# Kernel optimization log

Measured on AMD Instinct MI355X. Metric: run time of the kernel, lower is better.

The kernel has to match this reference:

```python
import jax, jax.numpy as jnp
import numpy as np
import math

B, T, C = 8, 1024, 512
H = 8
HD = C // H  # 64
MAX_REL = 64 + 4  # args.block_size + args.time_cond


def setup_inputs() -> dict:
    key = jax.random.key(0)
    ks = jax.random.split(key, 12)
    xavier = lambda k, shape: jax.random.uniform(
        k, shape, jnp.float32, -1.0, 1.0) * math.sqrt(6.0 / (shape[0] + shape[1]))
    return {
        "x": jax.random.normal(ks[0], (B, T, C), jnp.float32),
        "Wq": xavier(ks[1], (C, C)), "bq": jnp.zeros((C,), jnp.float32),
        "Wk": xavier(ks[2], (C, C)), "bk": jnp.zeros((C,), jnp.float32),
        "Wv": xavier(ks[3], (C, C)), "bv": jnp.zeros((C,), jnp.float32),
        "Wo": xavier(ks[4], (C, C)), "bo": jnp.zeros((C,), jnp.float32),
        "rel_k": xavier(ks[5], (2 * MAX_REL + 1, HD)),
        "rel_v": xavier(ks[6], (2 * MAX_REL + 1, HD)),
    }


def _rel_index(t):
    # clipped relative distance matrix, shifted to [0, 2*MAX_REL]
    r = jnp.arange(t)
    dist = jnp.clip(r[None, :] - r[:, None], -MAX_REL, MAX_REL)
    return dist + MAX_REL  # (T, T) int32


def reference(x, Wq, bq, Wk, bk, Wv, bv, Wo, bo, rel_k, rel_v):
    b, t, c = x.shape
    h, hd = H, HD
    q = x @ Wq + bq
    k = x @ Wk + bk
    v = x @ Wv + bv
    rq = q.reshape(b, t, h, hd).transpose(0, 2, 1, 3)  # (B,H,T,hd)
    rk = k.reshape(b, t, h, hd).transpose(0, 2, 1, 3)
    rv = v.reshape(b, t, h, hd).transpose(0, 2, 1, 3)

    idx = _rel_index(t)                 # (T,T)
    rk2 = rel_k[idx]                    # (T,T,hd)
    rv2 = rel_v[idx]                    # (T,T,hd)

    attn1 = jnp.einsum("bhqd,bhkd->bhqk", rq, rk)
    attn2 = jnp.einsum("bhqd,qkd->bhqk", rq, rk2)
    # NOTE: original scales by 1/sqrt(embed_dim) (k.size(-1) == C), not head_dim
    attn = jax.nn.softmax((attn1 + attn2) * (1.0 / math.sqrt(c)), axis=-1)

    w1 = jnp.einsum("bhqk,bhkd->bhqd", attn, rv)
    w2 = jnp.einsum("bhqk,qkd->bhqd", attn, rv2)
    out = (w1 + w2).transpose(0, 2, 1, 3).reshape(b, t, c)
    return out @ Wo + bo
```

## Files before the change

### kernel.cpp

```cpp
#include <hip/hip_runtime.h>
#include <stdint.h>

#define Bb 8
#define Tt 1024
#define Cc 512
#define Hh 8
#define HD 64
#define MREL 68
#define NR 137
#define NRP 160
#define SCALE 0.044194173824159216f
#define KSCL  0.063763016845703125f

typedef unsigned short u16;
typedef unsigned int u32;
using u16x4  = __attribute__((ext_vector_type(4))) u16;
using u16x8  = __attribute__((ext_vector_type(8))) u16;
using u32x4  = __attribute__((ext_vector_type(4))) u32;
using f32x4  = __attribute__((ext_vector_type(4))) float;
using f32x16 = __attribute__((ext_vector_type(16))) float;
using bf16x8 = __attribute__((ext_vector_type(8))) __bf16;

__device__ __forceinline__ u16 f2bf(float f) {
  u32 u = __builtin_bit_cast(u32, f);
  u += 0x7FFF + ((u >> 16) & 1);
  return (u16)(u >> 16);
}
__device__ __forceinline__ float bf2f(u16 v) {
  return __builtin_bit_cast(float, (u32)v << 16);
}
__device__ __forceinline__ bf16x8 as_bf8(u16x8 v) { return __builtin_bit_cast(bf16x8, v); }
__device__ __forceinline__ bf16x8 frag4(u32 w0, u32 w1, u32 w2, u32 w3) {
  u32x4 v = {w0, w1, w2, w3};
  return __builtin_bit_cast(bf16x8, v);
}
__device__ __forceinline__ float fexp2(float x) {
  float r; asm("v_exp_f32 %0, %1" : "=v"(r) : "v"(x)); return r;
}
__device__ __forceinline__ u32 cvtpk(float lo, float hi) {
  u32 r; asm("v_cvt_pk_bf16_f32 %0, %1, %2" : "=v"(r) : "v"(lo), "v"(hi)); return r;
}
__device__ __forceinline__ bf16x8 ldsplit(const u16* base) {
  u16x4 lo = *(const u16x4*)(base);
  u16x4 hi = *(const u16x4*)(base + 8);
  u16x8 r = {lo[0], lo[1], lo[2], lo[3], hi[0], hi[1], hi[2], hi[3]};
  return as_bf8(r);
}

#define MFMA16(a, b, c) __builtin_amdgcn_mfma_f32_16x16x32_bf16((a), (b), (c), 0, 0, 0)
#define MFMA32(a, b, c) __builtin_amdgcn_mfma_f32_32x32x16_bf16((a), (b), (c), 0, 0, 0)

__global__ __launch_bounds__(256) void relv_prep(
    const float* __restrict__ rel_v, u16* __restrict__ rvT)
{
  int i = blockIdx.x * 256 + threadIdx.x;
  if (i < HD * NRP) {
    int d = i / NRP, r = i - d * NRP;
    rvT[i] = (r < NR) ? f2bf(rel_v[r * HD + d]) : (u16)0;
  }
}

__global__ __launch_bounds__(256) void w_prep(
    const float* __restrict__ Wq, const float* __restrict__ Wk,
    const float* __restrict__ Wv, const float* __restrict__ Wo,
    u16* __restrict__ WqT, u16* __restrict__ WkT,
    u16* __restrict__ WvT, u16* __restrict__ WoT)
{
  const float* W = blockIdx.y == 0 ? Wq : blockIdx.y == 1 ? Wk
                  : blockIdx.y == 2 ? Wv : Wo;
  u16* WT = blockIdx.y == 0 ? WqT : blockIdx.y == 1 ? WkT
           : blockIdx.y == 2 ? WvT : WoT;
  int i = blockIdx.x * 256 + threadIdx.x;
  int n = i >> 7, k4 = (i & 127) * 4;
  u16x4 o;
  #pragma unroll
  for (int j = 0; j < 4; ++j) o[j] = f2bf(W[(size_t)(k4 + j) * Cc + n]);
  *(u16x4*)&WT[(size_t)n * Cc + k4] = o;
}

__global__ __launch_bounds__(256) void qkv_gemm(
    const float* __restrict__ x,
    const u16* __restrict__ WqT, const u16* __restrict__ WkT,
    const u16* __restrict__ WvT,
    const float* __restrict__ bq, const float* __restrict__ bk,
    const float* __restrict__ bv,
    u16* __restrict__ Qb, u16* __restrict__ Kb, u16* __restrict__ VTb)
{
  __shared__ u16 Xs[64][40];
  __shared__ u16 WTs[3][64][40];

  const u16* Wp[3] = {WqT, WkT, WvT};
  const float* bp[3] = {bq, bk, bv};

  const int tid = threadIdx.x;
  const int wv_ = tid >> 6;
  const int l   = tid & 63;
  const int lr  = l & 15, lg = l >> 4;
  const int m0  = blockIdx.x * 64;
  const int n0  = blockIdx.y * 64;
  const int srow = tid >> 2, scol = (tid & 3) * 8;

  f32x4 acc[3][4];
  #pragma unroll
  for (int a = 0; a < 3; ++a)
    #pragma unroll
    for (int b = 0; b < 4; ++b) acc[a][b] = (f32x4){0.f, 0.f, 0.f, 0.f};

  for (int k0 = 0; k0 < Cc; k0 += 32) {
    {
      const float* xp = x + (size_t)(m0 + srow) * Cc + k0 + scol;
      f32x4 v0 = *(const f32x4*)xp;
      f32x4 v1 = *(const f32x4*)(xp + 4);
      u16x8 o = {f2bf(v0[0]), f2bf(v0[1]), f2bf(v0[2]), f2bf(v0[3]),
                 f2bf(v1[0]), f2bf(v1[1]), f2bf(v1[2]), f2bf(v1[3])};
      *(u16x8*)&Xs[srow][scol] = o;
    }
    #pragma unroll
    for (int q3 = 0; q3 < 3; ++q3) {
      u16x8 w = *(const u16x8*)(Wp[q3] + (size_t)(n0 + srow) * Cc + k0 + scol);
      *(u16x8*)&WTs[q3][srow][scol] = w;
    }
    __syncthreads();

    bf16x8 a = as_bf8(*(const u16x8*)&Xs[wv_ * 16 + lr][lg * 8]);
    #pragma unroll
    for (int q3 = 0; q3 < 3; ++q3) {
      #pragma unroll
      for (int nt = 0; nt < 4; ++nt) {
        bf16x8 b = as_bf8(*(const u16x8*)&WTs[q3][nt * 16 + lr][lg * 8]);
        acc[q3][nt] = MFMA16(a, b, acc[q3][nt]);
      }
    }
    __syncthreads();
  }

  const int bidx = m0 >> 10;
  #pragma unroll
  for (int q3 = 0; q3 < 3; ++q3) {
    #pragma unroll
    for (int nt = 0; nt < 4; ++nt) {
      int n = n0 + nt * 16 + lr;
      int h = n >> 6, d = n & 63;
      float bias = bp[q3][n];
      #pragma unroll
      for (int i = 0; i < 4; ++i) {
        int m = m0 + wv_ * 16 + lg * 4 + i;
        int t = m & (Tt - 1);
        u16 o = f2bf(acc[q3][nt][i] + bias);
        size_t bh = (size_t)(bidx * Hh + h);
        if (q3 == 0)      Qb[(bh * Tt + t) * HD + d] = o;
        else if (q3 == 1) Kb[(bh * Tt + t) * HD + d] = o;
        else              VTb[(bh * HD + d) * Tt + t] = o;
      }
    }
  }
}

__global__ __launch_bounds__(256, 3) void attn_kernel(
    const u16* __restrict__ Qb, const u16* __restrict__ Kb,
    const u16* __restrict__ VTb, const u16* __restrict__ rvT,
    const float* __restrict__ rel_k,
    u16* __restrict__ AO)
{
  __shared__ u16 S2L[32][144];
  __shared__ u16 a2L[32][176];
  __shared__ float Obuf[32][64];
  __shared__ float red[3][4][32];
  __shared__ float rowrcp[32];

  const int tid = threadIdx.x;
  const int wv_ = tid >> 6, l = tid & 63;
  const int l31 = l & 31, hi = l >> 5;
  const int lr16 = l & 15, lg16 = l >> 4;
  const int bh = blockIdx.x;
  const int q0 = blockIdx.y * 32;
  const int bidx = bh >> 3, h = bh & 7;

  const u16* Qh = Qb  + (size_t)bh * Tt * HD;
  const u16* Kh = Kb  + (size_t)bh * Tt * HD;
  const u16* Vh = VTb + (size_t)bh * HD * Tt;

  for (int i = tid; i < 32 * 176 / 2; i += 256) ((u32*)a2L)[i] = 0;
  for (int i = tid; i < 32 * 64; i += 256) ((float*)Obuf)[i] = 0.f;

  #pragma unroll
  for (int h16 = 0; h16 < 2; ++h16) {
    bf16x8 aQ0 = as_bf8(*(const u16x8*)(Qh + (size_t)(q0 + h16 * 16 + lr16) * HD + lg16 * 8));
    bf16x8 aQ1 = as_bf8(*(const u16x8*)(Qh + (size_t)(q0 + h16 * 16 + lr16) * HD + 32 + lg16 * 8));
    for (int ct = wv_; ct < 9; ct += 4) {
      int r = ct * 16 + lr16;
      f32x4 acc = {0.f, 0.f, 0.f, 0.f};
      #pragma unroll
      for (int d0 = 0; d0 < 64; d0 += 32) {
        u16x8 bbits = {0, 0, 0, 0, 0, 0, 0, 0};
        if (r < NR) {
          f32x4 v0 = *(const f32x4*)(rel_k + (size_t)r * HD + d0 + lg16 * 8);
          f32x4 v1 = *(const f32x4*)(rel_k + (size_t)r * HD + d0 + lg16 * 8 + 4);
          bbits = (u16x8){f2bf(v0[0]), f2bf(v0[1]), f2bf(v0[2]), f2bf(v0[3]),
                          f2bf(v1[0]), f2bf(v1[1]), f2bf(v1[2]), f2bf(v1[3])};
        }
        acc = MFMA16(d0 ? aQ1 : aQ0, as_bf8(bbits), acc);
      }
      #pragma unroll
      for (int i = 0; i < 4; ++i)
        S2L[h16 * 16 + lg16 * 4 + i][ct * 16 + lr16] = f2bf(acc[i] * KSCL);
    }
  }
  __syncthreads();

  const int qme = q0 + l31;
  const float cN = bf2f(S2L[l31][0]);
  const float cP = bf2f(S2L[l31][NR - 1]);

  bf16x8 qf[4];
  #pragma unroll
  for (int s = 0; s < 4; ++s)
    qf[s] = as_bf8(*(const u16x8*)(Qh + (size_t)qme * HD + 16 * s + 8 * hi));

  const int wk0 = wv_ * 256;
  f32x16 oA = {}, oB = {};
  float ps = 0.f, ps0 = 0.f, bnd = 0.f;

  #pragma unroll
  for (int t = 0; t < 8; ++t) {
    const int kc0 = wk0 + 32 * t;
    bf16x8 kf[4];
    #pragma unroll
    for (int s = 0; s < 4; ++s)
      kf[s] = as_bf8(*(const u16x8*)(Kh + (size_t)(kc0 + l31) * HD + 16 * s + 8 * hi));

    f32x16 acc = {};
    #pragma unroll
    for (int s = 0; s < 4; ++s) acc = MFMA32(kf[s], qf[s], acc);

    float p[16];
    const bool isLow  = (kc0 <= q0 - 99);
    const bool isHigh = (kc0 >= q0 + 99);
    if (isLow | isHigh) {
      const float c = isLow ? cN : cP;
      #pragma unroll
      for (int r = 0; r < 16; ++r) p[r] = fexp2(fmaf(acc[r], KSCL, c));
      float s16 = ((p[0]+p[1])+(p[2]+p[3])) + ((p[4]+p[5])+(p[6]+p[7]))
                + ((p[8]+p[9])+(p[10]+p[11])) + ((p[12]+p[13])+(p[14]+p[15]));
      ps += s16;
      if (isLow) ps0 += s16;
    } else {
      #pragma unroll
      for (int r = 0; r < 16; ++r) {
        int kcoff = (r & 3) + 8 * (r >> 2) + 4 * hi;
        int dr = kc0 + kcoff - qme;
        int drc = dr < -MREL ? -MREL : (dr > MREL ? MREL : dr);
        float pe = fexp2(fmaf(acc[r], KSCL, bf2f(S2L[l31][drc + MREL])));
        p[r] = pe;
        ps += pe;
        if (dr <= -MREL) ps0 += pe;
        if (dr >= -67 && dr <= 67) { a2L[l31][dr + MREL] = f2bf(pe); bnd += pe; }
      }
    }

    bf16x8 paLo = frag4(cvtpk(p[0], p[1]),  cvtpk(p[2], p[3]),
                        cvtpk(p[4], p[5]),  cvtpk(p[6], p[7]));
    bf16x8 paHi = frag4(cvtpk(p[8], p[9]),  cvtpk(p[10], p[11]),
                        cvtpk(p[12], p[13]), cvtpk(p[14], p[15]));

    const u16* vA = Vh + (size_t)l31 * Tt;
    const u16* vB = Vh + (size_t)(32 + l31) * Tt;
    bf16x8 vA0 = ldsplit(vA + kc0 + 4 * hi);
    bf16x8 vA1 = ldsplit(vA + kc0 + 16 + 4 * hi);
    bf16x8 vB0 = ldsplit(vB + kc0 + 4 * hi);
    bf16x8 vB1 = ldsplit(vB + kc0 + 16 + 4 * hi);
    oA = MFMA32(paLo, vA0, oA);
    oA = MFMA32(paHi, vA1, oA);
    oB = MFMA32(paLo, vB0, oB);
    oB = MFMA32(paHi, vB1, oB);
  }

  ps  += __shfl_xor(ps, 32);
  ps0 += __shfl_xor(ps0, 32);
  bnd += __shfl_xor(bnd, 32);
  if (l < 32) { red[0][wv_][l] = ps; red[1][wv_][l] = ps0; red[2][wv_][l] = bnd; }
  __syncthreads();

  if (tid < 32) {
    float t0 = red[0][0][tid] + red[0][1][tid] + red[0][2][tid] + red[0][3][tid];
    float t1 = red[1][0][tid] + red[1][1][tid] + red[1][2][tid] + red[1][3][tid];
    float tb = red[2][0][tid] + red[2][1][tid] + red[2][2][tid] + red[2][3][tid];
    a2L[tid][0]      = f2bf(t1);
    a2L[tid][NR - 1] = f2bf(t0 - t1 - tb);
    rowrcp[tid] = 1.0f / t0;
  }
  __syncthreads();

  for (int W = wv_; W < 10; W += 4) {
    bf16x8 aa = as_bf8(*(const u16x8*)&a2L[l31][W * 16 + 8 * hi]);
    bf16x8 rA = as_bf8(*(const u16x8*)(rvT + (size_t)l31 * NRP        + W * 16 + 8 * hi));
    bf16x8 rB = as_bf8(*(const u16x8*)(rvT + (size_t)(32 + l31) * NRP + W * 16 + 8 * hi));
    oA = MFMA32(aa, rA, oA);
    oB = MFMA32(aa, rB, oB);
  }

  #pragma unroll
  for (int r = 0; r < 16; ++r) {
    int qoff = (r & 3) + 8 * (r >> 2) + 4 * hi;
    atomicAdd(&Obuf[qoff][l31], oA[r]);
    atomicAdd(&Obuf[qoff][32 + l31], oB[r]);
  }
  __syncthreads();

  {
    int rq = tid >> 3, d8 = (tid & 7) * 8;
    float rc = rowrcp[rq];
    u16x8 o;
    #pragma unroll
    for (int j = 0; j < 8; ++j) o[j] = f2bf(Obuf[rq][d8 + j] * rc);
    *(u16x8*)&AO[((size_t)(bidx * Tt + q0 + rq)) * Cc + h * HD + d8] = o;
  }
}

__global__ __launch_bounds__(256) void out_gemm(
    const u16* __restrict__ AO, const u16* __restrict__ WoT,
    const float* __restrict__ bo, float* __restrict__ out)
{
  __shared__ u16 As[64][40];
  __shared__ u16 WTs[64][40];
  const int tid = threadIdx.x;
  const int wv_ = tid >> 6, l = tid & 63, lr = l & 15, lg = l >> 4;
  const int m0 = blockIdx.x * 64, n0 = blockIdx.y * 64;
  const int srow = tid >> 2, scol = (tid & 3) * 8;

  f32x4 acc[4];
  #pragma unroll
  for (int b = 0; b < 4; ++b) acc[b] = (f32x4){0.f, 0.f, 0.f, 0.f};

  for (int k0 = 0; k0 < Cc; k0 += 32) {
    u16x8 av = *(const u16x8*)(AO + (size_t)(m0 + srow) * Cc + k0 + scol);
    *(u16x8*)&As[srow][scol] = av;
    u16x8 wv2 = *(const u16x8*)(WoT + (size_t)(n0 + srow) * Cc + k0 + scol);
    *(u16x8*)&WTs[srow][scol] = wv2;
    __syncthreads();

    bf16x8 a = as_bf8(*(const u16x8*)&As[wv_ * 16 + lr][lg * 8]);
    #pragma unroll
    for (int nt = 0; nt < 4; ++nt) {
      bf16x8 b = as_bf8(*(const u16x8*)&WTs[nt * 16 + lr][lg * 8]);
      acc[nt] = MFMA16(a, b, acc[nt]);
    }
    __syncthreads();
  }

  #pragma unroll
  for (int nt = 0; nt < 4; ++nt) {
    int n = n0 + nt * 16 + lr;
    float bias = bo[n];
    #pragma unroll
    for (int i = 0; i < 4; ++i) {
      int m = m0 + wv_ * 16 + lg * 4 + i;
      out[(size_t)m * Cc + n] = acc[nt][i] + bias;
    }
  }
}

extern "C" void kernel_launch(void* const* d_in, const int* in_sizes, int n_in,
                              void* d_out, int out_size, void* d_ws, size_t ws_size,
                              hipStream_t stream) {
  const float* x  = (const float*)d_in[0];
  const float* Wq = (const float*)d_in[1];
  const float* bq = (const float*)d_in[2];
  const float* Wk = (const float*)d_in[3];
  const float* bk = (const float*)d_in[4];
  const float* Wv = (const float*)d_in[5];
  const float* bv = (const float*)d_in[6];
  const float* Wo = (const float*)d_in[7];
  const float* bo = (const float*)d_in[8];
  const float* rk = (const float*)d_in[9];
  const float* rv = (const float*)d_in[10];

  const size_t BHTD = (size_t)Bb * Hh * Tt * HD;
  const size_t WSZ  = (size_t)Cc * Cc;

  u16* Qb = (u16*)d_out;
  u16* Kb = Qb + BHTD;
  u16* VT  = (u16*)d_ws;
  u16* AO  = VT + BHTD;
  u16* rvT = AO + BHTD;
  u16* WqT = rvT + (size_t)HD * NRP;
  u16* WkT = WqT + WSZ;
  u16* WvT = WkT + WSZ;
  u16* WoT = WvT + WSZ;
  float* outf = (float*)d_out;

  relv_prep<<<dim3((HD * NRP + 255) / 256), 256, 0, stream>>>(rv, rvT);
  w_prep<<<dim3(256, 4), 256, 0, stream>>>(Wq, Wk, Wv, Wo, WqT, WkT, WvT, WoT);
  qkv_gemm<<<dim3(128, 8), 256, 0, stream>>>(x, WqT, WkT, WvT, bq, bk, bv, Qb, Kb, VT);
  attn_kernel<<<dim3(64, 32), 256, 0, stream>>>(Qb, Kb, VT, rvT, rk, AO);
  out_gemm<<<dim3(128, 8), 256, 0, stream>>>(AO, WoT, bo, outf);
}
```

Before: 249.5 us.

## Permute V^T layout for 16-byte loads and software-pipeline K fragment loads

The projection kernel now writes V^T with a permuted time index within each 16-element group. This lets the attention kernel fetch each V fragment with a single 16-byte load instead of two 8-byte loads. The attention loop also prefetches the next K tile into registers and hoists V loads to the top of each iteration, so global latency overlaps the QK MFMAs and the softmax. The cost is extra register pressure from the double-buffered K fragments under launch_bounds(256,3). The V layout change also has to stay consistent with any other consumer of VTb.

```diff
diff --git a/kernel.cpp b/kernel.cpp
--- a/kernel.cpp
+++ b/kernel.cpp
@@ -40,15 +40,15 @@
 __device__ __forceinline__ u32 cvtpk(float lo, float hi) {
   u32 r; asm("v_cvt_pk_bf16_f32 %0, %1, %2" : "=v"(r) : "v"(lo), "v"(hi)); return r;
 }
-__device__ __forceinline__ bf16x8 ldsplit(const u16* base) {
-  u16x4 lo = *(const u16x4*)(base);
-  u16x4 hi = *(const u16x4*)(base + 8);
-  u16x8 r = {lo[0], lo[1], lo[2], lo[3], hi[0], hi[1], hi[2], hi[3]};
-  return as_bf8(r);
-}
 
 #define MFMA16(a, b, c) __builtin_amdgcn_mfma_f32_16x16x32_bf16((a), (b), (c), 0, 0, 0)
 #define MFMA32(a, b, c) __builtin_amdgcn_mfma_f32_32x32x16_bf16((a), (b), (c), 0, 0, 0)
+
+__device__ __forceinline__ int vperm(int t) {
+  int c = t & 15;
+  int cp = (c & 4) ? ((c & 8) ? c : c + 4) : ((c & 8) ? c - 4 : c);
+  return (t & ~15) | cp;
+}
 
 __global__ __launch_bounds__(256) void relv_prep(
     const float* __restrict__ rel_v, u16* __restrict__ rvT)
@@ -150,7 +150,7 @@
         size_t bh = (size_t)(bidx * Hh + h);
         if (q3 == 0)      Qb[(bh * Tt + t) * HD + d] = o;
         else if (q3 == 1) Kb[(bh * Tt + t) * HD + d] = o;
-        else              VTb[(bh * HD + d) * Tt + t] = o;
+        else              VTb[(bh * HD + d) * Tt + vperm(t)] = o;
       }
     }
   }
@@ -180,6 +180,14 @@
   const u16* Kh = Kb  + (size_t)bh * Tt * HD;
   const u16* Vh = VTb + (size_t)bh * HD * Tt;
 
+  const int wk0 = wv_ * 256;
+
+  const u16* kfp = Kh + (size_t)(wk0 + l31) * HD + 8 * hi;
+  bf16x8 kf[4], kn[4];
+  #pragma unroll
+  for (int s = 0; s < 4; ++s)
+    kf[s] = as_bf8(*(const u16x8*)(kfp + 16 * s));
+
   for (int i = tid; i < 32 * 176 / 2; i += 256) ((u32*)a2L)[i] = 0;
   for (int i = tid; i < 32 * 64; i += 256) ((float*)Obuf)[i] = 0.f;
 
@@ -217,17 +225,25 @@
   for (int s = 0; s < 4; ++s)
     qf[s] = as_bf8(*(const u16x8*)(Qh + (size_t)qme * HD + 16 * s + 8 * hi));
 
-  const int wk0 = wv_ * 256;
+  const u16* vAp = Vh + (size_t)l31 * Tt + 8 * hi;
+  const u16* vBp = Vh + (size_t)(32 + l31) * Tt + 8 * hi;
+
   f32x16 oA = {}, oB = {};
   float ps = 0.f, ps0 = 0.f, bnd = 0.f;
 
   #pragma unroll
   for (int t = 0; t < 8; ++t) {
     const int kc0 = wk0 + 32 * t;
-    bf16x8 kf[4];
-    #pragma unroll
-    for (int s = 0; s < 4; ++s)
-      kf[s] = as_bf8(*(const u16x8*)(Kh + (size_t)(kc0 + l31) * HD + 16 * s + 8 * hi));
+
+    bf16x8 vA0 = as_bf8(*(const u16x8*)(vAp + kc0));
+    bf16x8 vA1 = as_bf8(*(const u16x8*)(vAp + kc0 + 16));
+    bf16x8 vB0 = as_bf8(*(const u16x8*)(vBp + kc0));
+    bf16x8 vB1 = as_bf8(*(const u16x8*)(vBp + kc0 + 16));
+    if (t < 7) {
+      #pragma unroll
+      for (int s = 0; s < 4; ++s)
+        kn[s] = as_bf8(*(const u16x8*)(kfp + (size_t)(t + 1) * 32 * HD + 16 * s));
+    }
 
     f32x16 acc = {};
     #pragma unroll
@@ -263,16 +279,13 @@
     bf16x8 paHi = frag4(cvtpk(p[8], p[9]),  cvtpk(p[10], p[11]),
                         cvtpk(p[12], p[13]), cvtpk(p[14], p[15]));
 
-    const u16* vA = Vh + (size_t)l31 * Tt;
-    const u16* vB = Vh + (size_t)(32 + l31) * Tt;
-    bf16x8 vA0 = ldsplit(vA + kc0 + 4 * hi);
-    bf16x8 vA1 = ldsplit(vA + kc0 + 16 + 4 * hi);
-    bf16x8 vB0 = ldsplit(vB + kc0 + 4 * hi);
-    bf16x8 vB1 = ldsplit(vB + kc0 + 16 + 4 * hi);
     oA = MFMA32(paLo, vA0, oA);
     oA = MFMA32(paHi, vA1, oA);
     oB = MFMA32(paLo, vB0, oB);
     oB = MFMA32(paHi, vB1, oB);
+
+    #pragma unroll
+    for (int s = 0; s < 4; ++s) kf[s] = kn[s];
   }
 
   ps  += __shfl_xor(ps, 32);
```

Result: faster. 239.0 us (-4.2%).
